# Kernel optimization log

Hardware: AMD Instinct MI355X
Metric: run time of the kernel (lower is better)

The kernel has to match this reference:

```python
import jax, jax.numpy as jnp
import numpy as np

jax.config.update("jax_enable_x64", True)

POOL = np.array([4.0, 4.0, 4.0], dtype=np.float32)  # pool_size
N, E, D, B = 400_000, 3_200_000, 64, 16


def setup_inputs() -> dict:
    key = jax.random.key(0)
    k1, k2, k3, k4 = jax.random.split(key, 4)
    x = jax.random.normal(k1, (N, D), dtype=jnp.float32)
    pos = jax.random.uniform(k2, (N, 3), dtype=jnp.float32) * 128.0
    batch = jnp.sort(jax.random.randint(k3, (N,), 0, B)).astype(jnp.int64)
    edge_index = jax.random.randint(k4, (E, 2), 0, N).astype(jnp.int64)
    return {"x": x, "pos": pos, "edge_index": edge_index, "batch": batch}


def _voxel_key(pos, batch):
    # torch.div(pos, pool, rounding_mode='floor').long()
    qpos = jnp.floor(pos / jnp.asarray(POOL)).astype(jnp.int64)  # [N,3]
    strides = [int(qpos[:, i].max()) + 1 for i in range(3)]
    k = batch.astype(jnp.int64)
    for i in range(3):
        k = k * strides[i] + qpos[:, i]  # linearized (batch, qx, qy, qz) key
    return k, strides


def reference(x, pos, edge_index, batch):
    keyv, s = _voxel_key(pos, batch)
    ukey, inv = jnp.unique(keyv, return_inverse=True)  # unique voxel keys
    M = int(ukey.shape[0])
    new_batch = ukey // (s[0] * s[1] * s[2])  # recover batch id from key prefix

    # average_positions=True: scatter-mean of pos (include_self=False == pure mean)
    counts = jax.ops.segment_sum(jnp.ones((pos.shape[0],), pos.dtype), inv, num_segments=M)
    pos_mean = jax.ops.segment_sum(pos, inv, num_segments=M) / counts[:, None]

    # scatter-reduce amax of features (every segment non-empty by construction)
    pooled_x = jax.ops.segment_max(x, inv, num_segments=M)

    # remap edges, drop self-loops, dedup, append self-loops for all M nodes
    ei = inv[edge_index]  # [E,2]
    mask = ei[:, 0] != ei[:, 1]
    enc = ei[:, 0].astype(jnp.int64) * M + ei[:, 1].astype(jnp.int64)
    uenc = jnp.unique(enc[mask])
    ei_dedup = jnp.stack([uenc // M, uenc % M], axis=1)
    ar = jnp.arange(M, dtype=ei_dedup.dtype)
    loops = jnp.stack([ar, ar], axis=1)
    ei_out = jnp.concatenate([ei_dedup, loops], axis=0)

    return pooled_x, pos_mean, ei_out, new_batch
```

## Files before the change

kernel.cpp:

```cpp
#include <hip/hip_runtime.h>


#define KSP 524288
#define SCAN_BLOCK 256
#define SCAN_ITEMS 16
#define SCAN_CHUNK 4096
#define NCHUNK (KSP / SCAN_CHUNK)
#define NPART 2048
#define PSHIFT 8
#define PB 256
#define SCAP2 4096
#define NCOARSE 64
#define CSHIFT 13
#define CMASK 8191u
#define PS_ITERS 16


__global__ void k_keys(const float* __restrict__ pos, const int* __restrict__ batch,
                       unsigned* __restrict__ key, unsigned* __restrict__ cnt, int N) {
  int i = blockIdx.x * blockDim.x + threadIdx.x;
  if (i >= N) return;
  unsigned q0 = (unsigned)(int)floorf(pos[3 * i + 0] * 0.25f);
  unsigned q1 = (unsigned)(int)floorf(pos[3 * i + 1] * 0.25f);
  unsigned q2 = (unsigned)(int)floorf(pos[3 * i + 2] * 0.25f);
  unsigned k = ((((((unsigned)batch[i] << 5) | q0) << 5) | q1) << 5) | q2;
  key[i] = k;
  atomicAdd(&cnt[k], 1u);
}

__global__ void scanA2(const unsigned* __restrict__ in, unsigned* __restrict__ outRank,
                       unsigned* __restrict__ outStart, unsigned* __restrict__ chunkP,
                       unsigned* __restrict__ chunkC, int n) {
  __shared__ unsigned ldsP[SCAN_BLOCK];
  __shared__ unsigned ldsC[SCAN_BLOCK];
  int tbase = blockIdx.x * SCAN_CHUNK + threadIdx.x * SCAN_ITEMS;
  unsigned valsP[SCAN_ITEMS], valsC[SCAN_ITEMS];
  unsigned sp = 0, sc = 0;
  for (int i = 0; i < SCAN_ITEMS; ++i) {
    unsigned v = 0;
    int idx = tbase + i;
    if (idx < n) v = in[idx];
    valsP[i] = sp; valsC[i] = sc;
    sp += v ? 1u : 0u;
    sc += v;
  }
  ldsP[threadIdx.x] = sp; ldsC[threadIdx.x] = sc;
  __syncthreads();
  for (int off = 1; off < SCAN_BLOCK; off <<= 1) {
    unsigned tp = (threadIdx.x >= (unsigned)off) ? ldsP[threadIdx.x - off] : 0u;
    unsigned tc = (threadIdx.x >= (unsigned)off) ? ldsC[threadIdx.x - off] : 0u;
    __syncthreads();
    ldsP[threadIdx.x] += tp; ldsC[threadIdx.x] += tc;
    __syncthreads();
  }
  unsigned exP = ldsP[threadIdx.x] - sp;
  unsigned exC = ldsC[threadIdx.x] - sc;
  for (int i = 0; i < SCAN_ITEMS; ++i) {
    int idx = tbase + i;
    if (idx < n) { outRank[idx] = exP + valsP[i]; outStart[idx] = exC + valsC[i]; }
  }
  if (threadIdx.x == SCAN_BLOCK - 1) {
    chunkP[blockIdx.x] = ldsP[SCAN_BLOCK - 1];
    chunkC[blockIdx.x] = ldsC[SCAN_BLOCK - 1];
  }
}

__global__ void scanB2(unsigned* chunkP, unsigned* chunkC, unsigned* mDst) {
  __shared__ unsigned lp[NCHUNK];
  __shared__ unsigned lc[NCHUNK];
  unsigned t = threadIdx.x;
  unsigned vp = chunkP[t], vc = chunkC[t];
  lp[t] = vp; lc[t] = vc;
  __syncthreads();
  for (int off = 1; off < NCHUNK; off <<= 1) {
    unsigned xp = (t >= (unsigned)off) ? lp[t - off] : 0u;
    unsigned xc = (t >= (unsigned)off) ? lc[t - off] : 0u;
    __syncthreads();
    lp[t] += xp; lc[t] += xc;
    __syncthreads();
  }
  chunkP[t] = lp[t] - vp;
  chunkC[t] = lc[t] - vc;
  if (t == NCHUNK - 1 && mDst) *mDst = lp[NCHUNK - 1];
}

__global__ void scanC2(unsigned* __restrict__ rank, unsigned* __restrict__ ptStart,
                       const unsigned* __restrict__ chunkP, const unsigned* __restrict__ chunkC,
                       int n) {
  int idx = blockIdx.x * blockDim.x + threadIdx.x;
  if (idx >= n) return;
  int ch = idx / SCAN_CHUNK;
  rank[idx] += chunkP[ch];
  ptStart[idx] += chunkC[ch];
}

__global__ void k_scanP(const unsigned* __restrict__ in, unsigned* __restrict__ outStart,
                        unsigned* __restrict__ outCursor, unsigned* __restrict__ ccur,
                        unsigned* __restrict__ totalDst) {
  __shared__ unsigned lds[1024];
  unsigned t = threadIdx.x;
  unsigned a = in[2 * t], b = in[2 * t + 1];
  unsigned sum = a + b;
  lds[t] = sum;
  __syncthreads();
  for (int off = 1; off < 1024; off <<= 1) {
    unsigned x = (t >= (unsigned)off) ? lds[t - off] : 0u;
    __syncthreads();
    lds[t] += x;
    __syncthreads();
  }
  unsigned excl = lds[t] - sum;
  outStart[2 * t] = excl;
  outStart[2 * t + 1] = excl + a;
  if (outCursor) { outCursor[2 * t] = excl; outCursor[2 * t + 1] = excl + a; }
  if (ccur && (t & 15u) == 0) ccur[t >> 4] = excl;
  if (t == 1023) {
    outStart[NPART] = lds[1023];
    if (totalDst) *totalDst = lds[1023];
  }
}

__global__ void k_ukey(const unsigned* __restrict__ cnt, const unsigned* __restrict__ rank,
                       const unsigned* __restrict__ ptStart, const unsigned* __restrict__ hdr,
                       unsigned* __restrict__ ukeyArr, unsigned* __restrict__ cStart, int N) {
  int k = blockIdx.x * blockDim.x + threadIdx.x;
  if (k >= KSP) return;
  if (cnt[k]) {
    unsigned r = rank[k];
    ukeyArr[r] = (unsigned)k;
    cStart[r] = ptStart[k];
  }
  if (k == 0) cStart[hdr[3]] = (unsigned)N;
}

__global__ void k_scatter(const unsigned* __restrict__ key, const unsigned* __restrict__ rank,
                          unsigned* __restrict__ inv, unsigned* __restrict__ ptStart,
                          unsigned* __restrict__ ptOrder, int N) {
  int i = blockIdx.x * blockDim.x + threadIdx.x;
  if (i >= N) return;
  unsigned k = key[i];
  inv[i] = rank[k];
  unsigned posn = atomicAdd(&ptStart[k], 1u);
  ptOrder[posn] = (unsigned)i;
}

__global__ void __launch_bounds__(256) k_pool(const float4* __restrict__ x4,
                                              const float* __restrict__ pos,
                                              const unsigned* __restrict__ ptOrder,
                                              const unsigned* __restrict__ cStart,
                                              const unsigned* __restrict__ hdr,
                                              float* __restrict__ out) {
  unsigned gtid = blockIdx.x * blockDim.x + threadIdx.x;
  unsigned m = gtid >> 3;
  unsigned l = gtid & 7u;
  unsigned M = hdr[3];
  if (m >= M) return;
  unsigned start = cStart[m];
  unsigned n = cStart[m + 1] - start;
  const float NI = -__builtin_huge_valf();
  float4 a0 = make_float4(NI, NI, NI, NI);
  float4 a1 = a0;
  float psum = 0.0f;
  for (unsigned j = 0; j < n; ++j) {
    unsigned p = ptOrder[start + j];
    float4 v0 = x4[p * 16u + l];
    float4 v1 = x4[p * 16u + 8u + l];
    a0.x = fmaxf(a0.x, v0.x); a0.y = fmaxf(a0.y, v0.y);
    a0.z = fmaxf(a0.z, v0.z); a0.w = fmaxf(a0.w, v0.w);
    a1.x = fmaxf(a1.x, v1.x); a1.y = fmaxf(a1.y, v1.y);
    a1.z = fmaxf(a1.z, v1.z); a1.w = fmaxf(a1.w, v1.w);
    if (l < 3) psum += pos[3u * p + l];
  }
  float4* o4 = (float4*)out;
  o4[m * 16u + l] = a0;
  o4[m * 16u + 8u + l] = a1;
  if (l < 3) {
    unsigned long long O1 = 64ull * M;
    out[O1 + 3ull * m + l] = psum / (float)n;
  }
}

__global__ void __launch_bounds__(256) k_ehist2(const int2* __restrict__ ei,
                                                const unsigned* __restrict__ inv,
                                                unsigned* __restrict__ partCnt, int E, int span) {
  __shared__ unsigned h[NPART];
  for (int i = threadIdx.x; i < NPART; i += 256) h[i] = 0;
  __syncthreads();
  int lo = blockIdx.x * span;
  int hi = min(E, lo + span);
  for (int e = lo + threadIdx.x; e < hi; e += 256) {
    int2 pr = ei[e];
    unsigned a = inv[pr.x], b = inv[pr.y];
    if (a != b) atomicAdd(&h[a >> PSHIFT], 1u);
  }
  __syncthreads();
  for (int i = threadIdx.x; i < NPART; i += 256) {
    unsigned v = h[i];
    if (v) atomicAdd(&partCnt[i], v);
  }
}

__global__ void __launch_bounds__(256) k_pscat1(const int2* __restrict__ ei,
                                                const unsigned* __restrict__ inv,
                                                unsigned* __restrict__ ccur,
                                                unsigned* __restrict__ stage1, int E) {
  __shared__ unsigned h[NCOARSE];
  if (threadIdx.x < NCOARSE) h[threadIdx.x] = 0;
  __syncthreads();
  int lo = blockIdx.x * (256 * PS_ITERS);
  unsigned long long codes[PS_ITERS];
#pragma unroll
  for (int it = 0; it < PS_ITERS; ++it) {
    codes[it] = ~0ull;
    int e = lo + threadIdx.x + it * 256;
    if (e < E) {
      int2 pr = ei[e];
      unsigned a = inv[pr.x], b = inv[pr.y];
      if (a != b) {
        codes[it] = ((unsigned long long)a << 19) | b;
        atomicAdd(&h[a >> CSHIFT], 1u);
      }
    }
  }
  __syncthreads();
  if (threadIdx.x < NCOARSE) {
    unsigned v = h[threadIdx.x];
    h[threadIdx.x] = v ? atomicAdd(&ccur[threadIdx.x], v) : 0u;
  }
  __syncthreads();
#pragma unroll
  for (int it = 0; it < PS_ITERS; ++it) {
    unsigned long long code = codes[it];
    if (code != ~0ull) {
      unsigned a = (unsigned)(code >> 19);
      unsigned off = atomicAdd(&h[a >> CSHIFT], 1u);
      stage1[off] = ((a & CMASK) << 19) | ((unsigned)code & 0x7FFFFu);
    }
  }
}

__global__ void __launch_bounds__(256) k_pscat2(const unsigned* __restrict__ stage1,
                                                const unsigned* __restrict__ partStart,
                                                unsigned* __restrict__ partCursor,
                                                unsigned* __restrict__ pStage) {
  __shared__ unsigned h[NPART];
  __shared__ unsigned cbL[NCOARSE + 1];
  __shared__ unsigned c0s;
  for (int i = threadIdx.x; i < NPART; i += 256) h[i] = 0;
  if (threadIdx.x <= NCOARSE) cbL[threadIdx.x] = partStart[threadIdx.x << 5];
  __syncthreads();
  unsigned base = blockIdx.x * (256u * PS_ITERS);
  unsigned validE = cbL[NCOARSE];
  if (base >= validE) return;
  if (threadIdx.x == 0) {
    unsigned c = 0;
    while (cbL[c + 1] <= base) ++c;
    c0s = c;
  }
  __syncthreads();
  unsigned codes[PS_ITERS], prt[PS_ITERS];
  unsigned c = c0s;
#pragma unroll
  for (int it = 0; it < PS_ITERS; ++it) {
    prt[it] = 0xFFFFFFFFu;
    unsigned g = base + threadIdx.x + it * 256u;
    if (g < validE) {
      while (cbL[c + 1] <= g) ++c;
      unsigned code = stage1[g];
      codes[it] = code;
      unsigned part = (c << 5) | (code >> 27);
      prt[it] = part;
      atomicAdd(&h[part], 1u);
    }
  }
  __syncthreads();
  for (int i = threadIdx.x; i < NPART; i += 256) {
    unsigned v = h[i];
    h[i] = v ? atomicAdd(&partCursor[i], v) : 0u;
  }
  __syncthreads();
#pragma unroll
  for (int it = 0; it < PS_ITERS; ++it) {
    if (prt[it] != 0xFFFFFFFFu) {
      unsigned off = atomicAdd(&h[prt[it]], 1u);
      pStage[off] = codes[it] & 0x07FFFFFFu;
    }
  }
}

__global__ void __launch_bounds__(256) k_bucket(unsigned* __restrict__ pStage,
                                                const unsigned* __restrict__ partStart,
                                                unsigned* __restrict__ partDistinct) {
  __shared__ unsigned dstL[SCAP2];
  __shared__ unsigned h[PB];
  __shared__ unsigned bbase[PB + 1];
  __shared__ unsigned stmp[256];
  unsigned p = blockIdx.x;
  unsigned s = partStart[p];
  unsigned c = partStart[p + 1] - s;
  unsigned t = threadIdx.x;
  h[t] = 0;
  __syncthreads();
  if (c <= SCAP2) {
    const unsigned* src = pStage + s;
    for (unsigned i = t; i < c; i += 256) atomicAdd(&h[src[i] >> 19], 1u);
    __syncthreads();
    {
      unsigned v = h[t];
      stmp[t] = v;
      __syncthreads();
      for (int off = 1; off < 256; off <<= 1) {
        unsigned x = (t >= (unsigned)off) ? stmp[t - off] : 0u;
        __syncthreads(); stmp[t] += x; __syncthreads();
      }
      bbase[t] = stmp[t] - v;
      if (t == 255) bbase[PB] = stmp[255];
    }
    __syncthreads();
    h[t] = bbase[t];
    __syncthreads();
    for (unsigned i = t; i < c; i += 256) {
      unsigned code = src[i];
      unsigned off = atomicAdd(&h[code >> 19], 1u);
      dstL[off] = code;
    }
    __syncthreads();
    unsigned L = (c + 255) >> 8;
    unsigned vv[16], rr[16];
#pragma unroll
    for (unsigned k = 0; k < 16; ++k) {
      unsigned i = t * L + k;
      if (k < L && i < c) {
        unsigned v = dstL[i];
        unsigned b = v >> 19;
        unsigned blo = bbase[b], bhi = bbase[b + 1];
        unsigned r = blo;
        for (unsigned j = blo; j < bhi; ++j) {
          unsigned u = dstL[j];
          r += (u < v) || (u == v && j < i);
        }
        vv[k] = v; rr[k] = r;
      }
    }
    __syncthreads();
#pragma unroll
    for (unsigned k = 0; k < 16; ++k) {
      unsigned i = t * L + k;
      if (k < L && i < c) dstL[rr[k]] = vv[k];
    }
    __syncthreads();
    unsigned flm = 0, localSum = 0;
#pragma unroll
    for (unsigned k = 0; k < 16; ++k) {
      unsigned i = t * L + k;
      if (k < L && i < c) {
        unsigned v = dstL[i];
        unsigned pv = dstL[i - (i > 0 ? 1u : 0u)];
        unsigned f = (i == 0) | (pv != v);
        flm |= f << k;
        localSum += f;
      }
    }
    stmp[t] = localSum;
    __syncthreads();
    for (int off = 1; off < 256; off <<= 1) {
      unsigned x = (t >= (unsigned)off) ? stmp[t - off] : 0u;
      __syncthreads(); stmp[t] += x; __syncthreads();
    }
    unsigned pos = stmp[t] - localSum;
#pragma unroll
    for (unsigned k = 0; k < 16; ++k) {
      unsigned i = t * L + k;
      if (k < L && i < c && ((flm >> k) & 1u)) {
        pStage[s + pos] = dstL[i];
        ++pos;
      }
    }
    if (t == 255) partDistinct[p] = stmp[255];
  } else if (t == 0) {
    unsigned* a = pStage + s;
    for (unsigned i = 1; i < c; ++i) {
      unsigned v = a[i];
      long long j = (long long)i - 1;
      while (j >= 0 && a[j] > v) { a[j + 1] = a[j]; --j; }
      a[j + 1] = v;
    }
    unsigned d = 0, prev = 0xFFFFFFFFu;
    for (unsigned i = 0; i < c; ++i) {
      unsigned v = a[i];
      if (i == 0 || v != prev) { a[d] = v; ++d; }
      prev = v;
    }
    partDistinct[p] = d;
  }
}

__global__ void __launch_bounds__(256) k_ewriteP(const unsigned* __restrict__ pStage,
                                                 const unsigned* __restrict__ partStart,
                                                 const unsigned* __restrict__ partOut,
                                                 const unsigned* __restrict__ hdr,
                                                 float* __restrict__ out) {
  unsigned p = blockIdx.x;
  unsigned s = partStart[p];
  unsigned rbase = partOut[p];
  unsigned d = partOut[p + 1] - rbase;
  unsigned M = hdr[3];
  unsigned long long O2 = 67ull * M;
  unsigned pbase = p << PSHIFT;
  for (unsigned j = threadIdx.x; j < d; j += 256) {
    unsigned code = pStage[s + j];
    unsigned long long row = (unsigned long long)rbase + j;
    out[O2 + 2 * row + 0] = (float)(pbase | (code >> 19));
    out[O2 + 2 * row + 1] = (float)(code & 0x7FFFFu);
  }
}

__global__ void k_final(const unsigned* __restrict__ ukeyArr, const unsigned* __restrict__ hdr,
                        float* __restrict__ out) {
  unsigned m = blockIdx.x * blockDim.x + threadIdx.x;
  unsigned M = hdr[3];
  if (m >= M) return;
  unsigned Ed = hdr[5];
  unsigned long long O2 = 67ull * M;
  unsigned long long row = (unsigned long long)Ed + m;
  float fm = (float)m;
  out[O2 + 2 * row + 0] = fm;
  out[O2 + 2 * row + 1] = fm;
  unsigned long long O3 = O2 + 2ull * (Ed + M);
  out[O3 + m] = (float)(ukeyArr[m] >> 15);
}

extern "C" void kernel_launch(void* const* d_in, const int* in_sizes, int n_in,
                              void* d_out, int out_size, void* d_ws, size_t ws_size,
                              hipStream_t stream) {
  const float* x = (const float*)d_in[0];
  const float* pos = (const float*)d_in[1];
  const int* ei = (const int*)d_in[2];
  const int* batch = (const int*)d_in[3];
  float* out = (float*)d_out;
  int N = in_sizes[3];
  int E = in_sizes[2] / 2;

  unsigned* ws = (unsigned*)d_ws;
  unsigned* hdr          = ws;
  unsigned* cnt          = ws + 64;
  unsigned* partCnt      = cnt + KSP;
  unsigned* partDistinct = partCnt + NPART;
  unsigned* rank         = partDistinct + NPART;
  unsigned* ukeyArr      = rank + KSP;
  unsigned* cStart       = ukeyArr + KSP;
  unsigned* partStart    = cStart + KSP + 2;
  unsigned* partCursor   = partStart + NPART + 2;
  unsigned* partOut      = partCursor + NPART;
  unsigned* chunkP       = partOut + NPART + 2;
  unsigned* chunkC       = chunkP + 1024;
  unsigned* ccur         = chunkC + 1024;
  unsigned* key          = ccur + 66;
  unsigned* inv          = key + N;
  unsigned* pS32         = inv + ((N + 1) & ~1);
  unsigned* pStage       = pS32;
  unsigned* stage1       = pS32 + E;
  unsigned* ptStart  = pS32;
  unsigned* ptOrder  = pS32 + KSP;

  hipMemsetAsync(ws, 0, (size_t)(64 + KSP + 2 * NPART) * 4, stream);

  const int B = 256;
  int gN = (N + B - 1) / B;
  int gK = (KSP + B - 1) / B;
  int gP = (int)(((long long)N * 8 + B - 1) / B);
  int ebH = 2048;
  int spanH = (E + ebH - 1) / ebH;
  int ebS = (E + 256 * PS_ITERS - 1) / (256 * PS_ITERS);

  k_keys<<<gN, B, 0, stream>>>(pos, batch, key, cnt, N);

  scanA2<<<NCHUNK, SCAN_BLOCK, 0, stream>>>(cnt, rank, ptStart, chunkP, chunkC, KSP);
  scanB2<<<1, NCHUNK, 0, stream>>>(chunkP, chunkC, &hdr[3]);
  scanC2<<<gK, B, 0, stream>>>(rank, ptStart, chunkP, chunkC, KSP);

  k_ukey<<<gK, B, 0, stream>>>(cnt, rank, ptStart, hdr, ukeyArr, cStart, N);
  k_scatter<<<gN, B, 0, stream>>>(key, rank, inv, ptStart, ptOrder, N);
  k_pool<<<gP, B, 0, stream>>>((const float4*)x, pos, ptOrder, cStart, hdr, out);

  const int2* ei2 = (const int2*)ei;
  k_ehist2<<<ebH, 256, 0, stream>>>(ei2, inv, partCnt, E, spanH);
  k_scanP<<<1, 1024, 0, stream>>>(partCnt, partStart, partCursor, ccur, &hdr[4]);
  k_pscat1<<<ebS, 256, 0, stream>>>(ei2, inv, ccur, stage1, E);
  k_pscat2<<<ebS, 256, 0, stream>>>(stage1, partStart, partCursor, pStage);
  k_bucket<<<NPART, 256, 0, stream>>>(pStage, partStart, partDistinct);
  k_scanP<<<1, 1024, 0, stream>>>(partDistinct, partOut, nullptr, nullptr, &hdr[5]);
  k_ewriteP<<<NPART, 256, 0, stream>>>(pStage, partStart, partOut, hdr, out);
  k_final<<<gK, B, 0, stream>>>(ukeyArr, hdr, out);

  (void)n_in; (void)ws_size;
}
```

Measured before the change: 458.9 us.

## Defer self-loop filtering to bucket dedup so edge histogram reads only sources

The partition histogram now gathers only the source endpoint through inv, with loads batched per thread across 16 iterations, instead of gathering both endpoints to test for self-loops. Self-loops are kept through the partition scatter and removed later during per-partition dedup, where a packed code's low bits are compared with its reconstructed source id. This halves the random inv gathers in the histogram pass and raises memory-level parallelism, in exchange for sorting and carrying self-loop edges through the bucket stage.

```diff
diff --git a/kernel.cpp b/kernel.cpp
--- a/kernel.cpp
+++ b/kernel.cpp
@@ -180,18 +180,26 @@
   }
 }
 
-__global__ void __launch_bounds__(256) k_ehist2(const int2* __restrict__ ei,
-                                                const unsigned* __restrict__ inv,
-                                                unsigned* __restrict__ partCnt, int E, int span) {
+__global__ void __launch_bounds__(256) k_ehist(const int2* __restrict__ ei,
+                                               const unsigned* __restrict__ inv,
+                                               unsigned* __restrict__ partCnt, int E) {
   __shared__ unsigned h[NPART];
   for (int i = threadIdx.x; i < NPART; i += 256) h[i] = 0;
   __syncthreads();
-  int lo = blockIdx.x * span;
-  int hi = min(E, lo + span);
-  for (int e = lo + threadIdx.x; e < hi; e += 256) {
-    int2 pr = ei[e];
-    unsigned a = inv[pr.x], b = inv[pr.y];
-    if (a != b) atomicAdd(&h[a >> PSHIFT], 1u);
+  int lo = blockIdx.x * (256 * PS_ITERS);
+  unsigned av[PS_ITERS];
+#pragma unroll
+  for (int it = 0; it < PS_ITERS; ++it) {
+    int e = lo + threadIdx.x + it * 256;
+    av[it] = (e < E) ? (unsigned)ei[e].x : 0xFFFFFFFFu;
+  }
+#pragma unroll
+  for (int it = 0; it < PS_ITERS; ++it) {
+    if (av[it] != 0xFFFFFFFFu) av[it] = inv[av[it]];
+  }
+#pragma unroll
+  for (int it = 0; it < PS_ITERS; ++it) {
+    if (av[it] != 0xFFFFFFFFu) atomicAdd(&h[av[it] >> PSHIFT], 1u);
   }
   __syncthreads();
   for (int i = threadIdx.x; i < NPART; i += 256) {
@@ -216,10 +224,8 @@
     if (e < E) {
       int2 pr = ei[e];
       unsigned a = inv[pr.x], b = inv[pr.y];
-      if (a != b) {
-        codes[it] = ((unsigned long long)a << 19) | b;
-        atomicAdd(&h[a >> CSHIFT], 1u);
-      }
+      codes[it] = ((unsigned long long)a << 19) | b;
+      atomicAdd(&h[a >> CSHIFT], 1u);
     }
   }
   __syncthreads();
@@ -299,6 +305,7 @@
   unsigned s = partStart[p];
   unsigned c = partStart[p + 1] - s;
   unsigned t = threadIdx.x;
+  unsigned pb = p << PSHIFT;
   h[t] = 0;
   __syncthreads();
   if (c <= SCAP2) {
@@ -356,7 +363,8 @@
       if (k < L && i < c) {
         unsigned v = dstL[i];
         unsigned pv = dstL[i - (i > 0 ? 1u : 0u)];
-        unsigned f = (i == 0) | (pv != v);
+        unsigned notself = ((v & 0x7FFFFu) != (pb | (v >> 19))) ? 1u : 0u;
+        unsigned f = (((i == 0) | (pv != v)) ? 1u : 0u) & notself;
         flm |= f << k;
         localSum += f;
       }
@@ -388,7 +396,7 @@
     unsigned d = 0, prev = 0xFFFFFFFFu;
     for (unsigned i = 0; i < c; ++i) {
       unsigned v = a[i];
-      if (i == 0 || v != prev) { a[d] = v; ++d; }
+      if ((i == 0 || v != prev) && ((v & 0x7FFFFu) != (pb | (v >> 19)))) { a[d] = v; ++d; }
       prev = v;
     }
     partDistinct[p] = d;
@@ -469,8 +477,6 @@
   int gN = (N + B - 1) / B;
   int gK = (KSP + B - 1) / B;
   int gP = (int)(((long long)N * 8 + B - 1) / B);
-  int ebH = 2048;
-  int spanH = (E + ebH - 1) / ebH;
   int ebS = (E + 256 * PS_ITERS - 1) / (256 * PS_ITERS);
 
   k_keys<<<gN, B, 0, stream>>>(pos, batch, key, cnt, N);
@@ -484,7 +490,7 @@
   k_pool<<<gP, B, 0, stream>>>((const float4*)x, pos, ptOrder, cStart, hdr, out);
 
   const int2* ei2 = (const int2*)ei;
-  k_ehist2<<<ebH, 256, 0, stream>>>(ei2, inv, partCnt, E, spanH);
+  k_ehist<<<ebS, 256, 0, stream>>>(ei2, inv, partCnt, E);
   k_scanP<<<1, 1024, 0, stream>>>(partCnt, partStart, partCursor, ccur, &hdr[4]);
   k_pscat1<<<ebS, 256, 0, stream>>>(ei2, inv, ccur, stage1, E);
   k_pscat2<<<ebS, 256, 0, stream>>>(stage1, partStart, partCursor, pStage);
```

New measurement: 430.5 us. 1.07x faster.
